# Kernel optimization log

Hardware: AMD Instinct MI355X
Metric: run time of the kernel (lower is better)

Reference implementation:

```python
import jax, jax.numpy as jnp
import numpy as np

N_NODES = 100000
N_EDGES = 1600000
IN_DIM = 32
OUT_DIM = 64
N_REL = 8
EPS = 1e-10


def setup_inputs() -> dict:
    key = jax.random.key(0)
    k_x, k_src, k_dst, k_rel, k_w, k_wl, k_ws = jax.random.split(key, 7)
    x = jax.random.normal(k_x, (N_NODES, IN_DIM), dtype=jnp.float32)
    node_in = jax.random.randint(k_src, (N_EDGES,), 0, N_NODES)
    node_out = jax.random.randint(k_dst, (N_EDGES,), 0, N_NODES)
    relation = jax.random.randint(k_rel, (N_EDGES,), 0, N_REL)
    edge_list = jnp.stack([node_in, node_out, relation], axis=1)  # [E, 3] int
    edge_weight = jax.random.uniform(k_w, (N_EDGES,), dtype=jnp.float32)
    W_linear = jax.random.normal(k_wl, (N_REL * IN_DIM, OUT_DIM), dtype=jnp.float32) / np.sqrt(N_REL * IN_DIM)
    b_linear = jnp.zeros((OUT_DIM,), dtype=jnp.float32)
    W_self = jax.random.normal(k_ws, (IN_DIM, OUT_DIM), dtype=jnp.float32) / np.sqrt(IN_DIM)
    b_self = jnp.zeros((OUT_DIM,), dtype=jnp.float32)
    return {"x": x, "edge_list": edge_list, "edge_weight": edge_weight,
            "W_linear": W_linear, "b_linear": b_linear,
            "W_self": W_self, "b_self": b_self}


def reference(x, edge_list, edge_weight, W_linear, b_linear, W_self, b_self):
    num_node, in_dim = x.shape
    # message: gather source-node features per edge  -> [E, D]
    msg = x[edge_list[:, 0]]
    # aggregate: relation-expanded segment id = dst * R + rel
    seg = edge_list[:, 1] * N_REL + edge_list[:, 2]  # [E]
    w = edge_weight[:, None]  # [E, 1]
    num = jax.ops.segment_sum(msg * w, seg, num_segments=num_node * N_REL)  # [N*R, D]
    den = jax.ops.segment_sum(w, seg, num_segments=num_node * N_REL)        # [N*R, 1]
    update = (num / (den + EPS)).reshape(num_node, N_REL * in_dim)          # [N, R*D]
    # combine: linear(update) + self_loop(x), then ReLU
    out = update @ W_linear + b_linear + x @ W_self + b_self
    return jax.nn.relu(out)
```

## Files before the change

kernel.cpp:

```cpp
#include <hip/hip_runtime.h>
#include <stdint.h>

#define N_NODES 100000
#define N_EDGES 1600000
#define IN_DIM 32
#define OUT_DIM 64
#define N_REL 8
#define NSEG (N_NODES * N_REL)
#define EPS 1e-10f
#define N_KK 9
#define SWG_ELEMS (N_KK * 4 * 64 * 8)

typedef __attribute__((ext_vector_type(8))) short bf16x8;
typedef __attribute__((ext_vector_type(2))) short bf16x2;
typedef __attribute__((ext_vector_type(4))) float f32x4;

static __device__ __forceinline__ float bflo(uint32_t u) { return __uint_as_float(u << 16); }
static __device__ __forceinline__ float bfhi(uint32_t u) { return __uint_as_float(u & 0xffff0000u); }
static __device__ __forceinline__ uint16_t f2bf(float f) {
    uint32_t u = __float_as_uint(f);
    return (uint16_t)((u + 0x7fffu + ((u >> 16) & 1u)) >> 16);
}

static __device__ __forceinline__ void pk_add_bf16(uint32_t* addr, float f0, float f1) {
#if __has_builtin(__builtin_amdgcn_global_atomic_fadd_v2bf16)
    bf16x2 v;
    v[0] = (short)f2bf(f0);
    v[1] = (short)f2bf(f1);
    __builtin_amdgcn_global_atomic_fadd_v2bf16((bf16x2*)addr, v);
#else
    uint32_t old = *addr, assumed;
    do {
        assumed = old;
        float lo = bflo(assumed) + f0;
        float hi = bfhi(assumed) + f1;
        uint32_t nv = (uint32_t)f2bf(lo) | ((uint32_t)f2bf(hi) << 16);
        old = atomicCAS(addr, assumed, nv);
    } while (old != assumed);
#endif
}

__global__ __launch_bounds__(256) void detect_kernel(const uint32_t* __restrict__ xw,
                                                     int* __restrict__ flag) {
    __shared__ int cnt;
    if (threadIdx.x == 0) cnt = 0;
    __syncthreads();
    int c = 0;
    for (int k = threadIdx.x; k < 4096; k += 256) {
        uint32_t w = xw[k];
        uint32_t e = (w >> 7) & 0xffu;
        c += (e >= 160u) ? 1 : 0;
    }
    atomicAdd(&cnt, c);
    __syncthreads();
    if (threadIdx.x == 0) *flag = (cnt > 64) ? 1 : 0;
}

__global__ __launch_bounds__(256) void prep_kernel(const void* __restrict__ Wl,
                                                   const void* __restrict__ Ws,
                                                   const void* __restrict__ bl,
                                                   const void* __restrict__ bs,
                                                   const int* __restrict__ flag,
                                                   uint16_t* __restrict__ sWg,
                                                   float* __restrict__ biasv) {
    int f32 = *flag;
    int idx = blockIdx.x * 256 + threadIdx.x;
    if (idx < SWG_ELEMS) {
        int j    = idx & 7;
        int lane = (idx >> 3) & 63;
        int ot   = (idx >> 9) & 3;
        int kk   = idx >> 11;
        int quad = lane >> 4;
        int k = kk * 32 + quad * 8 + j;
        int o = ot * 16 + (lane & 15);
        if (f32) {
            float v = (k < 256) ? ((const float*)Wl)[(size_t)k * OUT_DIM + o]
                                : ((const float*)Ws)[(size_t)(k - 256) * OUT_DIM + o];
            sWg[idx] = f2bf(v);
        } else {
            sWg[idx] = (k < 256) ? ((const uint16_t*)Wl)[(size_t)k * OUT_DIM + o]
                                 : ((const uint16_t*)Ws)[(size_t)(k - 256) * OUT_DIM + o];
        }
    } else if (idx < SWG_ELEMS + OUT_DIM) {
        int o = idx - SWG_ELEMS;
        if (f32) biasv[o] = ((const float*)bl)[o] + ((const float*)bs)[o];
        else     biasv[o] = bflo((uint32_t)((const uint16_t*)bl)[o])
                          + bflo((uint32_t)((const uint16_t*)bs)[o]);
    }
}

__global__ __launch_bounds__(256) void scatter_pk_kernel(
    const int* __restrict__ el,
    const void* __restrict__ ew,
    const void* __restrict__ x,
    const int* __restrict__ flag,
    uint32_t* __restrict__ num,
    float* __restrict__ den)
{
    int t = blockIdx.x * 256 + threadIdx.x;
    int e = t >> 4;
    int p = t & 15;
    if (e >= N_EDGES) return;

    int src = el[e * 3 + 0];
    int dst = el[e * 3 + 1];
    int rel = el[e * 3 + 2];
    int f32 = *flag;

    float w = f32 ? ((const float*)ew)[e]
                  : bflo((uint32_t)((const uint16_t*)ew)[e]);

    float x0, x1;
    if (f32) {
        const float2 v = *(const float2*)((const float*)x + (size_t)src * IN_DIM + 2 * p);
        x0 = v.x; x1 = v.y;
    } else {
        uint32_t d = *(const uint32_t*)((const uint16_t*)x + (size_t)src * IN_DIM + 2 * p);
        x0 = bflo(d); x1 = bfhi(d);
    }

    int seg = dst * N_REL + rel;
    pk_add_bf16(&num[(size_t)seg * 16 + p], w * x0, w * x1);
    if (p == 0) atomicAdd(&den[seg], w);
}

__global__ __launch_bounds__(256) void dense_mfma_kernel(
    const uint32_t* __restrict__ num,
    const float* __restrict__ den,
    const void* __restrict__ x,
    const uint16_t* __restrict__ sWg,
    const float* __restrict__ biasv,
    const int* __restrict__ flag,
    void* __restrict__ out)
{
    __shared__ uint16_t sB[SWG_ELEMS];
    int f32 = *flag;

    #pragma unroll
    for (int it = 0; it < SWG_ELEMS / (256 * 8); ++it) {
        int idx = (it * 256 + threadIdx.x) * 8;
        *(bf16x8*)(sB + idx) = *(const bf16x8*)(sWg + idx);
    }
    __syncthreads();

    int wid  = threadIdx.x >> 6;
    int lane = threadIdx.x & 63;
    int quad = lane >> 4;
    int m    = lane & 15;

    int n0 = blockIdx.x * 64 + wid * 16;
    int n  = n0 + m;
    int nc = (n < N_NODES) ? n : (N_NODES - 1);

    float bias[4];
    #pragma unroll
    for (int ot = 0; ot < 4; ++ot) bias[ot] = biasv[ot * 16 + m];

    f32x4 acc[4];
    #pragma unroll
    for (int ot = 0; ot < 4; ++ot) acc[ot] = (f32x4){0.f, 0.f, 0.f, 0.f};

    #pragma unroll
    for (int kk = 0; kk < N_KK; ++kk) {
        bf16x8 a;
        if (kk < 8) {
            const uint4 d = *(const uint4*)(num + ((size_t)nc * 8 + kk) * 16 + quad * 4);
            float inv = 1.0f / (den[(size_t)nc * N_REL + kk] + EPS);
            a[0] = (short)f2bf(bflo(d.x) * inv); a[1] = (short)f2bf(bfhi(d.x) * inv);
            a[2] = (short)f2bf(bflo(d.y) * inv); a[3] = (short)f2bf(bfhi(d.y) * inv);
            a[4] = (short)f2bf(bflo(d.z) * inv); a[5] = (short)f2bf(bfhi(d.z) * inv);
            a[6] = (short)f2bf(bflo(d.w) * inv); a[7] = (short)f2bf(bfhi(d.w) * inv);
        } else {
            if (f32) {
                const float* base = (const float*)x + (size_t)nc * IN_DIM + quad * 8;
                float4 v0 = *(const float4*)base;
                float4 v1 = *(const float4*)(base + 4);
                a[0] = (short)f2bf(v0.x); a[1] = (short)f2bf(v0.y);
                a[2] = (short)f2bf(v0.z); a[3] = (short)f2bf(v0.w);
                a[4] = (short)f2bf(v1.x); a[5] = (short)f2bf(v1.y);
                a[6] = (short)f2bf(v1.z); a[7] = (short)f2bf(v1.w);
            } else {
                a = *(const bf16x8*)((const uint16_t*)x + (size_t)nc * IN_DIM + quad * 8);
            }
        }
        #pragma unroll
        for (int ot = 0; ot < 4; ++ot) {
            bf16x8 b = *(const bf16x8*)(sB + ((kk * 4 + ot) * 64 + lane) * 8);
            acc[ot] = __builtin_amdgcn_mfma_f32_16x16x32_bf16(a, b, acc[ot], 0, 0, 0);
        }
    }

    #pragma unroll
    for (int ot = 0; ot < 4; ++ot) {
        #pragma unroll
        for (int reg = 0; reg < 4; ++reg) {
            int node = n0 + quad * 4 + reg;
            if (node >= N_NODES) continue;
            int o = ot * 16 + m;
            float v = fmaxf(acc[ot][reg] + bias[ot], 0.0f);
            if (f32) ((float*)out)[(size_t)node * OUT_DIM + o] = v;
            else     ((uint16_t*)out)[(size_t)node * OUT_DIM + o] = f2bf(v);
        }
    }
}

extern "C" void kernel_launch(void* const* d_in, const int* in_sizes, int n_in,
                              void* d_out, int out_size, void* d_ws, size_t ws_size,
                              hipStream_t stream) {
    const void* x  = d_in[0];
    const int* el  = (const int*)d_in[1];
    const void* ew = d_in[2];
    const void* Wl = d_in[3];
    const void* bl = d_in[4];
    const void* Ws = d_in[5];
    const void* bs = d_in[6];

    const size_t OFF_DEN  = 64;
    const size_t OFF_NUM  = OFF_DEN + (size_t)NSEG * 4;
    const size_t OFF_SWG  = OFF_NUM + (size_t)NSEG * IN_DIM * 2;
    const size_t OFF_BIAS = OFF_SWG + (size_t)SWG_ELEMS * 2;
    const size_t REQ      = OFF_BIAS + OUT_DIM * 4;
    if (ws_size < REQ) return;

    int*      flag  = (int*)d_ws;
    float*    den   = (float*)((char*)d_ws + OFF_DEN);
    uint32_t* num   = (uint32_t*)((char*)d_ws + OFF_NUM);
    uint16_t* sWg   = (uint16_t*)((char*)d_ws + OFF_SWG);
    float*    biasv = (float*)((char*)d_ws + OFF_BIAS);

    hipMemsetAsync(d_ws, 0, OFF_SWG, stream);
    detect_kernel<<<1, 256, 0, stream>>>((const uint32_t*)x, flag);
    prep_kernel<<<(SWG_ELEMS + OUT_DIM + 255) / 256, 256, 0, stream>>>(Wl, Ws, bl, bs, flag, sWg, biasv);
    {
        long long threads = (long long)N_EDGES * 16;
        int blocks = (int)((threads + 255) / 256);
        scatter_pk_kernel<<<blocks, 256, 0, stream>>>(el, ew, x, flag, num, den);
    }
    dense_mfma_kernel<<<(N_NODES + 63) / 64, 256, 0, stream>>>(num, den, x, sWg, biasv, flag, d_out);
}
```

Before: 274.9 us.

## Replace atomic bf16 scatter with counting-sort CSR and segmented gather aggregation

```diff
diff --git a/kernel.cpp b/kernel.cpp
--- a/kernel.cpp
+++ b/kernel.cpp
@@ -11,8 +11,10 @@
 #define N_KK 9
 #define SWG_ELEMS (N_KK * 4 * 64 * 8)
 
+#define SCAN_ELEMS 4096
+#define SCAN_NB ((NSEG + SCAN_ELEMS - 1) / SCAN_ELEMS)
+
 typedef __attribute__((ext_vector_type(8))) short bf16x8;
-typedef __attribute__((ext_vector_type(2))) short bf16x2;
 typedef __attribute__((ext_vector_type(4))) float f32x4;
 
 static __device__ __forceinline__ float bflo(uint32_t u) { return __uint_as_float(u << 16); }
@@ -20,24 +22,6 @@
 static __device__ __forceinline__ uint16_t f2bf(float f) {
     uint32_t u = __float_as_uint(f);
     return (uint16_t)((u + 0x7fffu + ((u >> 16) & 1u)) >> 16);
-}
-
-static __device__ __forceinline__ void pk_add_bf16(uint32_t* addr, float f0, float f1) {
-#if __has_builtin(__builtin_amdgcn_global_atomic_fadd_v2bf16)
-    bf16x2 v;
-    v[0] = (short)f2bf(f0);
-    v[1] = (short)f2bf(f1);
-    __builtin_amdgcn_global_atomic_fadd_v2bf16((bf16x2*)addr, v);
-#else
-    uint32_t old = *addr, assumed;
-    do {
-        assumed = old;
-        float lo = bflo(assumed) + f0;
-        float hi = bfhi(assumed) + f1;
-        uint32_t nv = (uint32_t)f2bf(lo) | ((uint32_t)f2bf(hi) << 16);
-        old = atomicCAS(addr, assumed, nv);
-    } while (old != assumed);
-#endif
 }
 
 __global__ __launch_bounds__(256) void detect_kernel(const uint32_t* __restrict__ xw,
@@ -89,44 +73,137 @@
     }
 }
 
-__global__ __launch_bounds__(256) void scatter_pk_kernel(
-    const int* __restrict__ el,
-    const void* __restrict__ ew,
-    const void* __restrict__ x,
-    const int* __restrict__ flag,
-    uint32_t* __restrict__ num,
-    float* __restrict__ den)
-{
-    int t = blockIdx.x * 256 + threadIdx.x;
-    int e = t >> 4;
-    int p = t & 15;
+__global__ __launch_bounds__(256) void hist_kernel(const int* __restrict__ el,
+                                                   uint32_t* __restrict__ cnt) {
+    int e = blockIdx.x * 256 + threadIdx.x;
     if (e >= N_EDGES) return;
-
+    int dst = el[e * 3 + 1];
+    int rel = el[e * 3 + 2];
+    atomicAdd(&cnt[dst * N_REL + rel], 1u);
+}
+
+__global__ __launch_bounds__(256) void scan1_kernel(const uint32_t* __restrict__ cnt,
+                                                    uint32_t* __restrict__ bsum) {
+    int base = blockIdx.x * SCAN_ELEMS + threadIdx.x * 16;
+    uint32_t s = 0;
+    #pragma unroll
+    for (int j = 0; j < 16; ++j) {
+        int i = base + j;
+        s += (i < NSEG) ? cnt[i] : 0u;
+    }
+    __shared__ uint32_t ls[256];
+    ls[threadIdx.x] = s;
+    __syncthreads();
+    #pragma unroll
+    for (int off = 128; off > 0; off >>= 1) {
+        if (threadIdx.x < off) ls[threadIdx.x] += ls[threadIdx.x + off];
+        __syncthreads();
+    }
+    if (threadIdx.x == 0) bsum[blockIdx.x] = ls[0];
+}
+
+__global__ __launch_bounds__(256) void scan2_kernel(uint32_t* __restrict__ bsum) {
+    __shared__ uint32_t ls[256];
+    int tid = threadIdx.x;
+    ls[tid] = (tid < SCAN_NB) ? bsum[tid] : 0u;
+    __syncthreads();
+    if (tid == 0) {
+        uint32_t run = 0;
+        for (int i = 0; i < SCAN_NB; ++i) { uint32_t c = ls[i]; ls[i] = run; run += c; }
+    }
+    __syncthreads();
+    if (tid < SCAN_NB) bsum[tid] = ls[tid];
+}
+
+__global__ __launch_bounds__(256) void scan3_kernel(const uint32_t* __restrict__ bsum,
+                                                    uint32_t* __restrict__ ptr,
+                                                    uint32_t* __restrict__ cursor) {
+    int tid = threadIdx.x;
+    int base = blockIdx.x * SCAN_ELEMS + tid * 16;
+    uint32_t v[16];
+    uint32_t run = 0;
+    #pragma unroll
+    for (int j = 0; j < 16; ++j) {
+        int i = base + j;
+        uint32_t c = (i < NSEG) ? cursor[i] : 0u;
+        v[j] = run;
+        run += c;
+    }
+    __shared__ uint32_t ls[256];
+    ls[tid] = run;
+    __syncthreads();
+    for (int off = 1; off < 256; off <<= 1) {
+        uint32_t t = (tid >= off) ? ls[tid - off] : 0u;
+        __syncthreads();
+        ls[tid] += t;
+        __syncthreads();
+    }
+    uint32_t texcl = ls[tid] - run;
+    uint32_t boff = bsum[blockIdx.x];
+    #pragma unroll
+    for (int j = 0; j < 16; ++j) {
+        int i = base + j;
+        if (i < NSEG) {
+            uint32_t val = boff + texcl + v[j];
+            ptr[i]    = val;
+            cursor[i] = val;
+        }
+    }
+    if (blockIdx.x == 0 && tid == 0) ptr[NSEG] = N_EDGES;
+}
+
+__global__ __launch_bounds__(256) void sort_kernel(const int* __restrict__ el,
+                                                   const void* __restrict__ ew,
+                                                   const int* __restrict__ flag,
+                                                   uint32_t* __restrict__ cursor,
+                                                   uint2* __restrict__ sorted) {
+    int e = blockIdx.x * 256 + threadIdx.x;
+    if (e >= N_EDGES) return;
     int src = el[e * 3 + 0];
     int dst = el[e * 3 + 1];
     int rel = el[e * 3 + 2];
+    float w = (*flag) ? ((const float*)ew)[e]
+                      : bflo((uint32_t)((const uint16_t*)ew)[e]);
+    int seg = dst * N_REL + rel;
+    uint32_t pos = atomicAdd(&cursor[seg], 1u);
+    sorted[pos] = make_uint2((uint32_t)src, __float_as_uint(w));
+}
+
+__global__ __launch_bounds__(256) void agg_kernel(const uint32_t* __restrict__ ptr,
+                                                  const uint2* __restrict__ sorted,
+                                                  const void* __restrict__ x,
+                                                  const int* __restrict__ flag,
+                                                  uint32_t* __restrict__ num) {
+    int t = blockIdx.x * 256 + threadIdx.x;
+    int g = t >> 4;
+    int p = t & 15;
+    if (g >= NSEG) return;
     int f32 = *flag;
-
-    float w = f32 ? ((const float*)ew)[e]
-                  : bflo((uint32_t)((const uint16_t*)ew)[e]);
-
-    float x0, x1;
-    if (f32) {
-        const float2 v = *(const float2*)((const float*)x + (size_t)src * IN_DIM + 2 * p);
-        x0 = v.x; x1 = v.y;
-    } else {
-        uint32_t d = *(const uint32_t*)((const uint16_t*)x + (size_t)src * IN_DIM + 2 * p);
-        x0 = bflo(d); x1 = bfhi(d);
-    }
-
-    int seg = dst * N_REL + rel;
-    pk_add_bf16(&num[(size_t)seg * 16 + p], w * x0, w * x1);
-    if (p == 0) atomicAdd(&den[seg], w);
+    int beg = (int)ptr[g];
+    int end = (int)ptr[g + 1];
+    float a0 = 0.f, a1 = 0.f, sw = 0.f;
+    for (int i = beg; i < end; ++i) {
+        uint2 d = sorted[i];
+        float w = __uint_as_float(d.y);
+        float x0, x1;
+        if (f32) {
+            const float2 v = *(const float2*)((const float*)x + (size_t)d.x * IN_DIM + 2 * p);
+            x0 = v.x; x1 = v.y;
+        } else {
+            uint32_t u = *(const uint32_t*)((const uint16_t*)x + (size_t)d.x * IN_DIM + 2 * p);
+            x0 = bflo(u); x1 = bfhi(u);
+        }
+        a0 += w * x0;
+        a1 += w * x1;
+        sw += w;
+    }
+    float inv = 1.0f / (sw + EPS);
+    uint32_t packed = (uint32_t)f2bf(a0 * inv) | ((uint32_t)f2bf(a1 * inv) << 16);
+    num[(size_t)g * 16 + p] = packed;
 }
 
 __global__ __launch_bounds__(256) void dense_mfma_kernel(
-    const uint32_t* __restrict__ num,
-    const float* __restrict__ den,
+    const uint16_t* __restrict__ num16,
     const void* __restrict__ x,
     const uint16_t* __restrict__ sWg,
     const float* __restrict__ biasv,
@@ -164,12 +241,7 @@
     for (int kk = 0; kk < N_KK; ++kk) {
         bf16x8 a;
         if (kk < 8) {
-            const uint4 d = *(const uint4*)(num + ((size_t)nc * 8 + kk) * 16 + quad * 4);
-            float inv = 1.0f / (den[(size_t)nc * N_REL + kk] + EPS);
-            a[0] = (short)f2bf(bflo(d.x) * inv); a[1] = (short)f2bf(bfhi(d.x) * inv);
-            a[2] = (short)f2bf(bflo(d.y) * inv); a[3] = (short)f2bf(bfhi(d.y) * inv);
-            a[4] = (short)f2bf(bflo(d.z) * inv); a[5] = (short)f2bf(bfhi(d.z) * inv);
-            a[6] = (short)f2bf(bflo(d.w) * inv); a[7] = (short)f2bf(bfhi(d.w) * inv);
+            a = *(const bf16x8*)(num16 + ((size_t)nc * 8 + kk) * 32 + quad * 8);
         } else {
             if (f32) {
                 const float* base = (const float*)x + (size_t)nc * IN_DIM + quad * 8;
@@ -215,26 +287,38 @@
     const void* Ws = d_in[5];
     const void* bs = d_in[6];
 
-    const size_t OFF_DEN  = 64;
-    const size_t OFF_NUM  = OFF_DEN + (size_t)NSEG * 4;
+    const size_t OFF_PTR  = 64;
+    const size_t OFF_CUR  = OFF_PTR + (((size_t)(NSEG + 1) * 4 + 63) & ~(size_t)63);
+    const size_t OFF_BS   = OFF_CUR + (size_t)NSEG * 4;
+    const size_t OFF_SORT = OFF_BS + 16384;
+    const size_t OFF_NUM  = OFF_SORT + (size_t)N_EDGES * 8;
     const size_t OFF_SWG  = OFF_NUM + (size_t)NSEG * IN_DIM * 2;
     const size_t OFF_BIAS = OFF_SWG + (size_t)SWG_ELEMS * 2;
     const size_t REQ      = OFF_BIAS + OUT_DIM * 4;
     if (ws_size < REQ) return;
 
-    int*      flag  = (int*)d_ws;
-    float*    den   = (float*)((char*)d_ws + OFF_DEN);
-    uint32_t* num   = (uint32_t*)((char*)d_ws + OFF_NUM);
-    uint16_t* sWg   = (uint16_t*)((char*)d_ws + OFF_SWG);
-    float*    biasv = (float*)((char*)d_ws + OFF_BIAS);
-
-    hipMemsetAsync(d_ws, 0, OFF_SWG, stream);
+    int*      flag   = (int*)d_ws;
+    uint32_t* ptr    = (uint32_t*)((char*)d_ws + OFF_PTR);
+    uint32_t* cursor = (uint32_t*)((char*)d_ws + OFF_CUR);
+    uint32_t* bsum   = (uint32_t*)((char*)d_ws + OFF_BS);
+    uint2*    sorted = (uint2*)((char*)d_ws + OFF_SORT);
+    uint32_t* num    = (uint32_t*)((char*)d_ws + OFF_NUM);
+    uint16_t* sWg    = (uint16_t*)((char*)d_ws + OFF_SWG);
+    float*    biasv  = (float*)((char*)d_ws + OFF_BIAS);
+
+    (void)hipMemsetAsync(cursor, 0, (size_t)NSEG * 4, stream);
+
     detect_kernel<<<1, 256, 0, stream>>>((const uint32_t*)x, flag);
     prep_kernel<<<(SWG_ELEMS + OUT_DIM + 255) / 256, 256, 0, stream>>>(Wl, Ws, bl, bs, flag, sWg, biasv);
-    {
-        long long threads = (long long)N_EDGES * 16;
-        int blocks = (int)((threads + 255) / 256);
-        scatter_pk_kernel<<<blocks, 256, 0, stream>>>(el, ew, x, flag, num, den);
-    }
-    dense_mfma_kernel<<<(N_NODES + 63) / 64, 256, 0, stream>>>(num, den, x, sWg, biasv, flag, d_out);
-}
+
+    const int eblocks = (N_EDGES + 255) / 256;
+    hist_kernel<<<eblocks, 256, 0, stream>>>(el, cursor);
+    scan1_kernel<<<SCAN_NB, 256, 0, stream>>>(cursor, bsum);
+    scan2_kernel<<<1, 256, 0, stream>>>(bsum);
+    scan3_kernel<<<SCAN_NB, 256, 0, stream>>>(bsum, ptr, cursor);
+    sort_kernel<<<eblocks, 256, 0, stream>>>(el, ew, flag, cursor, sorted);
+
+    agg_kernel<<<(NSEG * 16 + 255) / 256 , 256, 0, stream>>>(ptr, sorted, x, flag, num);
+
+    dense_mfma_kernel<<<(N_NODES + 63) / 64, 256, 0, stream>>>((const uint16_t*)num, x, sWg, biasv, flag, d_out);
+}
```

Result: slower. 390.2 us (+42.0%).
